# Kernel optimization log

Measured on AMD Instinct MI355X. Metric: run time of the kernel, lower is better.

## Reference

```python
import jax, jax.numpy as jnp
import numpy as np
from jax import lax

B, C, H, W = 2, 64, 192, 192
KS = 3
N = KS * KS
L = 3  # num_gdns (ResBlocks)


def conv2d(x, w, b=None, padding=0):
    out = lax.conv_general_dilated(x, w, (1, 1), [(padding, padding)] * 2,
                                   dimension_numbers=('NCHW', 'OIHW', 'NCHW'))
    if b is not None:
        out = out + b[None, :, None, None]
    return out


def gdn(x, beta, gamma):
    # y = x / sqrt(beta + sum_j gamma_ij x_j^2)  (inverse=False)
    norm = conv2d(x * x, gamma[:, :, None, None], beta)
    return x / jnp.sqrt(norm)


def resblock(x, w1, w2, beta, gamma):
    res = x
    h = jax.nn.celu(gdn(conv2d(x, w1, padding=0), beta, gamma))  # conv1: no pad (H-2)
    return conv2d(h, w2, padding=2) + res  # conv2: pad 2 restores H


def deform_conv(x, offset, w_dc):
    # DCNv1 (pure-pytorch impl): offset (b,2N,h,w), rows first then cols.
    b, c, Hh, Ww = x.shape
    h, w = offset.shape[2], offset.shape[3]
    pad = 1
    xp = jnp.pad(x, ((0, 0), (0, 0), (pad, pad), (pad, pad)))
    Hp, Wp = Hh + 2 * pad, Ww + 2 * pad
    r = (KS - 1) // 2
    knr, knc = jnp.meshgrid(jnp.arange(-r, r + 1), jnp.arange(-r, r + 1), indexing='ij')
    p_n = jnp.concatenate([knr.reshape(-1), knc.reshape(-1)]).astype(x.dtype)  # (2N,)
    gr, gc = jnp.meshgrid(jnp.arange(1, h + 1), jnp.arange(1, w + 1), indexing='ij')
    p0 = jnp.concatenate([jnp.broadcast_to(gr[None], (N, h, w)),
                          jnp.broadcast_to(gc[None], (N, h, w))], 0).astype(x.dtype)  # (2N,h,w)
    p = p0[None] + p_n[None, :, None, None] + offset  # (b,2N,h,w)
    p = jnp.transpose(p, (0, 2, 3, 1))  # (b,h,w,2N)
    pr = jnp.clip(p[..., :N], 0, Hp - 1)
    pc = jnp.clip(p[..., N:], 0, Wp - 1)
    q0 = lax.stop_gradient(jnp.floor(p))
    qr0 = jnp.clip(q0[..., :N], 0, Hp - 1).astype(jnp.int32)
    qc0 = jnp.clip(q0[..., N:], 0, Wp - 1).astype(jnp.int32)
    qr1 = jnp.clip(q0[..., :N] + 1, 0, Hp - 1).astype(jnp.int32)
    qc1 = jnp.clip(q0[..., N:] + 1, 0, Wp - 1).astype(jnp.int32)
    # bilinear weights (match torch impl exactly)
    g_lt = (1 + (qr0 - pr)) * (1 + (qc0 - pc))
    g_rb = (1 - (qr1 - pr)) * (1 - (qc1 - pc))
    g_lb = (1 + (qr0 - pr)) * (1 - (qc1 - pc))
    g_rt = (1 - (qr1 - pr)) * (1 + (qc0 - pc))
    xf = xp.reshape(b, c, Hp * Wp)

    def gather(qr, qc):
        idx = (qr * Wp + qc).reshape(b, -1)  # (b, h*w*N)
        g = jax.vmap(lambda xb, ib: xb[:, ib])(xf, idx)  # (b,c,h*w*N)
        return g.reshape(b, c, h, w, N)

    xo = (g_lt[:, None] * gather(qr0, qc0) + g_rb[:, None] * gather(qr1, qc1)
          + g_lb[:, None] * gather(qr0, qc1) + g_rt[:, None] * gather(qr1, qc0))
    # stride-ks conv over reshaped x_offset == contraction over (c, n)
    wf = w_dc.reshape(w_dc.shape[0], c, N)
    return jnp.einsum('bchwn,ocn->bohw', xo, wf)


def setup_inputs() -> dict:
    key = jax.random.key(0)
    ks = jax.random.split(key, 11)
    f_r = jax.random.normal(ks[0], (B, C, H, W), jnp.float32)
    m_t = jax.random.normal(ks[1], (B, C, H, W), jnp.float32)
    w_pconv = jax.random.normal(ks[2], (2 * N, C, KS, KS), jnp.float32) * 0.01
    b_pconv = jax.random.normal(ks[3], (2 * N,), jnp.float32) * 0.01
    w_dc = jax.random.normal(ks[4], (C, C, KS, KS), jnp.float32) * 0.05
    w_cat = jax.random.normal(ks[5], (C, 2 * C, KS, KS), jnp.float32) * 0.05
    b_cat = jax.random.normal(ks[6], (C,), jnp.float32) * 0.05
    rb_w1 = jax.random.normal(ks[7], (L, C, C, KS, KS), jnp.float32) * 0.01
    rb_w2 = jax.random.normal(ks[8], (L, C, C, KS, KS), jnp.float32) * 0.01
    rb_beta = jax.random.uniform(ks[9], (L, C), jnp.float32) * 0.5 + 0.5
    rb_gamma = jnp.broadcast_to(0.1 * jnp.eye(C, dtype=jnp.float32), (L, C, C)) \
        + jax.random.uniform(ks[10], (L, C, C), jnp.float32) * 0.01
    return {"f_r": f_r, "m_t": m_t, "w_pconv": w_pconv, "b_pconv": b_pconv,
            "w_dc": w_dc, "w_cat": w_cat, "b_cat": b_cat,
            "rb_w1": rb_w1, "rb_w2": rb_w2, "rb_beta": rb_beta, "rb_gamma": rb_gamma}


def reference(f_r, m_t, w_pconv, b_pconv, w_dc, w_cat, b_cat, rb_w1, rb_w2, rb_beta, rb_gamma):
    offset = conv2d(m_t, w_pconv, b_pconv, padding=1)  # (B, 2N, H, W)
    x = deform_conv(f_r, offset, w_dc)                  # (B, C, H, W)
    y = conv2d(jnp.concatenate([x, f_r], axis=1), w_cat, b_cat, padding=1)
    for i in range(L):
        y = resblock(y, rb_w1[i], rb_w2[i], rb_beta[i], rb_gamma[i])
    return y + x
```

## Files before the change

kernel.cpp:

```cpp
#include <hip/hip_runtime.h>

typedef __attribute__((ext_vector_type(8))) __bf16 bf16x8;
typedef __attribute__((ext_vector_type(4))) __bf16 bf16x4;
typedef __attribute__((ext_vector_type(16))) float f32x16;
typedef __attribute__((ext_vector_type(4))) float f32x4;
typedef __attribute__((ext_vector_type(4))) int i32x4;

#define HH 192
#define WW 192
#define HW 36864
#define HW1 36100

#define TCS 144
#define RP66 (66 * TCS)
#define RPA (34 * TCS)
#define RPB (36 * TCS)
#define LDSA (4 * RPA)
#define LDSB (6 * RPB)
#define GDNPITCH 144
#define TREG 8704

__device__ inline f32x16 mfma32(bf16x8 a, bf16x8 b, f32x16 c) {
  return __builtin_amdgcn_mfma_f32_32x32x16_bf16(a, b, c, 0, 0, 0);
}

__device__ inline f32x16 zero16() {
  f32x16 z;
#pragma unroll
  for (int e = 0; e < 16; ++e) z[e] = 0.f;
  return z;
}

__global__ __launch_bounds__(256) void prep_weights(
    const float* __restrict__ wp, const float* __restrict__ bp,
    const float* __restrict__ wdc, const float* __restrict__ wcat,
    const float* __restrict__ w1, const float* __restrict__ w2,
    const float* __restrict__ gamma,
    __bf16* __restrict__ wpA, __bf16* __restrict__ wdcA,
    __bf16* __restrict__ wcatA, __bf16* __restrict__ w1A,
    __bf16* __restrict__ w2A, __bf16* __restrict__ gA,
    float* __restrict__ bpad) {
  int i = blockIdx.x * 256 + threadIdx.x;
  if (i < 18432) {
    int j = i & 7, lane = (i >> 3) & 63, kc = (i >> 9) & 3, n = i >> 11;
    int o = lane & 31, c = kc * 16 + ((lane >> 5) << 3) + j;
    wpA[i] = (o < 18) ? (__bf16)wp[(o * 64 + c) * 9 + n] : (__bf16)0.f;
    return;
  }
  i -= 18432;
  if (i < 36864) {
    int j = i & 7, lane = (i >> 3) & 63, ot = (i >> 9) & 1, kc = (i >> 10) & 3, n = i >> 12;
    int o = ot * 32 + (lane & 31), c = kc * 16 + ((lane >> 5) << 3) + j;
    wdcA[i] = (__bf16)wdc[(o * 64 + c) * 9 + n];
    return;
  }
  i -= 36864;
  if (i < 73728) {
    int d = i, j = d & 7; d >>= 3; int lane = d & 63; d >>= 6; int ot = d & 1; d >>= 1;
    int kc = d & 7; int n = d >> 3;
    int o = ot * 32 + (lane & 31), c = kc * 16 + ((lane >> 5) << 3) + j;
    wcatA[i] = (__bf16)wcat[(o * 128 + c) * 9 + n];
    return;
  }
  i -= 73728;
  if (i < 110592) {
    int l = i / 36864, di = i % 36864, d = di;
    int j = d & 7; d >>= 3; int lane = d & 63; d >>= 6; int ot = d & 1; d >>= 1;
    int kc = d & 3; int n = d >> 2;
    int o = ot * 32 + (lane & 31), c = kc * 16 + ((lane >> 5) << 3) + j;
    w1A[l * 36864 + di] = (__bf16)w1[l * 36864 + (o * 64 + c) * 9 + n];
    return;
  }
  i -= 110592;
  if (i < 110592) {
    int l = i / 36864, di = i % 36864, d = di;
    int j = d & 7; d >>= 3; int lane = d & 63; d >>= 6; int ot = d & 1; d >>= 1;
    int kc = d & 3; int n = d >> 2;
    int o = ot * 32 + (lane & 31), c = kc * 16 + ((lane >> 5) << 3) + j;
    w2A[l * 36864 + di] = (__bf16)w2[l * 36864 + (o * 64 + c) * 9 + n];
    return;
  }
  i -= 110592;
  if (i < 12288) {
    int l = i / 4096, di = i % 4096, d = di;
    int j = d & 7; d >>= 3; int lane = d & 63; d >>= 6; int ot = d & 1; d >>= 1;
    int kc = d & 3;
    int o = ot * 32 + (lane & 31), c = kc * 16 + ((lane >> 5) << 3) + j;
    gA[l * 4096 + di] = (__bf16)gamma[l * 4096 + o * 64 + c];
    return;
  }
  i -= 12288;
  if (i < 20) bpad[i] = (i < 18) ? bp[i] : 0.f;
}

__global__ __launch_bounds__(256) void to_nhwc_bf16(
    const float* __restrict__ fr, const float* __restrict__ mt,
    __bf16* __restrict__ frn, __bf16* __restrict__ mtn) {
  __shared__ __align__(16) __bf16 tile[64 * 72];
  int tensor = blockIdx.x / 1152, rem = blockIdx.x % 1152;
  int b = rem / 576, p0 = (rem % 576) * 64;
  const float* src = (tensor ? mt : fr) + (size_t)b * 64 * HW;
  __bf16* dst = (tensor ? mtn : frn) + (size_t)b * HW * 64;
  int tid = threadIdx.x, c = tid >> 2, q0 = (tid & 3) * 16;
  const float* sp = src + (size_t)c * HW + p0 + q0;
#pragma unroll
  for (int qq = 0; qq < 4; ++qq) {
    f32x4 v = *(const f32x4*)(sp + qq * 4);
#pragma unroll
    for (int e = 0; e < 4; ++e) tile[(q0 + qq * 4 + e) * 72 + c] = (__bf16)v[e];
  }
  __syncthreads();
  int px = tid >> 2, c0 = (tid & 3) * 16;
  bf16x8 a = *(const bf16x8*)(&tile[px * 72 + c0]);
  bf16x8 b8 = *(const bf16x8*)(&tile[px * 72 + c0 + 8]);
  __bf16* dp = dst + (size_t)(p0 + px) * 64 + c0;
  *(bf16x8*)dp = a;
  *(bf16x8*)(dp + 8) = b8;
}

template <int ROWS, int COLS, int TPB>
__device__ inline void stage_f32T(const float* __restrict__ src,
                                  int srcH, int srcW, int row0, int col0,
                                  unsigned char* lds) {
  for (int i = threadIdx.x; i < ROWS * COLS * 16; i += TPB) {
    int r = i / (COLS * 16), rem = i - r * (COLS * 16), j = rem >> 4, q = rem & 15;
    int gr = row0 + r, gc = col0 + j;
    f32x4 v = {0.f, 0.f, 0.f, 0.f};
    if (gr >= 0 && gr < srcH && gc >= 0 && gc < srcW)
      v = *(const f32x4*)(src + ((size_t)gr * srcW + gc) * 64 + q * 4);
    bf16x4 o;
#pragma unroll
    for (int e = 0; e < 4; ++e) o[e] = (__bf16)v[e];
    *(bf16x4*)(lds + r * (COLS * TCS) + j * TCS + q * 8) = o;
  }
}

template <int ROWS, int COLS, int TPB>
__device__ inline void stage_bf16T(const __bf16* __restrict__ src,
                                   int srcH, int srcW, int row0, int col0,
                                   unsigned char* lds) {
  for (int i = threadIdx.x; i < ROWS * COLS * 8; i += TPB) {
    int r = i / (COLS * 8), rem = i - r * (COLS * 8), j = rem >> 3, u = rem & 7;
    int gr = row0 + r, gc = col0 + j;
    bf16x8 v;
#pragma unroll
    for (int e = 0; e < 8; ++e) v[e] = (__bf16)0.f;
    if (gr >= 0 && gr < srcH && gc >= 0 && gc < srcW)
      v = *(const bf16x8*)(src + ((size_t)gr * srcW + gc) * 64 + u * 8);
    *(bf16x8*)(lds + r * (COLS * TCS) + j * TCS + u * 16) = v;
  }
}

template <int KC, int KOFFA, int RP>
__device__ inline void kloopW(const __bf16* __restrict__ wA,
                              const unsigned char* __restrict__ bB,
                              int ot, f32x16 acc2[2]) {
  const int lane = threadIdx.x & 63;
  const __bf16* aB = wA + lane * 8;
#pragma unroll
  for (int n = 0; n < 9; ++n) {
    const int kh = n / 3, kw = n % 3;
#pragma unroll
    for (int kc = 0; kc < 4; ++kc) {
      bf16x8 a = *(const bf16x8*)(aB + ((n * KC + KOFFA + kc) * 2 + ot) * 512);
      bf16x8 b0 = *(const bf16x8*)(bB + kh * RP + kw * TCS + kc * 32);
      acc2[kc & 1] = mfma32(a, b0, acc2[kc & 1]);
    }
  }
}

__device__ inline void acc32_to_lds(const f32x16 acc[2], unsigned char* reg) {
  int lane = threadIdx.x & 63;
  int colb = lane & 31, half = lane >> 5;
#pragma unroll
  for (int ot = 0; ot < 2; ++ot)
#pragma unroll
    for (int g = 0; g < 4; ++g) {
      int o = ot * 32 + half * 4 + g * 8;
      f32x4 v;
      v[0] = acc[ot][g * 4 + 0]; v[1] = acc[ot][g * 4 + 1];
      v[2] = acc[ot][g * 4 + 2]; v[3] = acc[ot][g * 4 + 3];
      *(f32x4*)(reg + (colb * 68 + o) * 4) = v;
    }
}

__global__ __launch_bounds__(256, 1) void pconv_mfma(
    const __bf16* __restrict__ mtn, const __bf16* __restrict__ wpA,
    const float* __restrict__ bpad, float* __restrict__ off20) {
  __shared__ __align__(16) unsigned char smem[6 * RP66];
  int b = blockIdx.x / 144, r = blockIdx.x % 144, rt = r / 3, ct = r % 3;
  int h0 = rt * 4, w0 = ct * 64;
  int wid = threadIdx.x >> 6, lane = threadIdx.x & 63;
  int colb = lane & 31, half = lane >> 5, kh8 = half << 3;
  stage_bf16T<6, 66, 256>(mtn + (size_t)b * HW * 64, 192, 192, h0 - 1, w0 - 1, smem);
  const __bf16* aB = wpA + lane * 8;
  bf16x8 pcur[4], pnxt[4];
#pragma unroll
  for (int kc = 0; kc < 4; ++kc) pcur[kc] = *(const bf16x8*)(aB + kc * 512);
  __syncthreads();
  f32x16 acc[2];
  acc[0] = zero16(); acc[1] = zero16();
  {
    const unsigned char* bB = smem + wid * RP66 + colb * TCS + kh8 * 2;
#pragma unroll
    for (int n = 0; n < 9; ++n) {
      if (n < 8) {
#pragma unroll
        for (int kc = 0; kc < 4; ++kc)
          pnxt[kc] = *(const bf16x8*)(aB + ((n + 1) * 4 + kc) * 512);
      }
      const int kh = n / 3, kw = n % 3;
#pragma unroll
      for (int kc = 0; kc < 4; ++kc) {
        const unsigned char* bp = bB + kh * RP66 + kw * TCS + kc * 32;
        bf16x8 b0 = *(const bf16x8*)(bp);
        bf16x8 b1 = *(const bf16x8*)(bp + 32 * TCS);
        acc[0] = mfma32(pcur[kc], b0, acc[0]);
        acc[1] = mfma32(pcur[kc], b1, acc[1]);
      }
#pragma unroll
      for (int kc = 0; kc < 4; ++kc) pcur[kc] = pnxt[kc];
    }
  }
  __syncthreads();
  unsigned char* reg = smem + wid * 9216;
#pragma unroll
  for (int pt = 0; pt < 2; ++pt)
#pragma unroll
    for (int g = 0; g < 4; ++g) {
      int o = half * 4 + g * 8;
      f32x4 v;
      v[0] = acc[pt][g * 4 + 0]; v[1] = acc[pt][g * 4 + 1];
      v[2] = acc[pt][g * 4 + 2]; v[3] = acc[pt][g * 4 + 3];
      *(f32x4*)(reg + ((pt * 32 + colb) * 36 + o) * 4) = v;
    }
  __builtin_amdgcn_s_waitcnt(0);
  size_t pix = (size_t)b * HW + (size_t)(h0 + wid) * 192 + w0 + lane;
#pragma unroll
  for (int q = 0; q < 5; ++q) {
    f32x4 v = *(const f32x4*)(reg + (lane * 36 + q * 4) * 4);
    v += *(const f32x4*)(bpad + q * 4);
    *(f32x4*)(off20 + pix * 20 + q * 4) = v;
  }
}

#define GOPITCH 32
#define DTBL (9 * 32 * GOPITCH)
#define DBUF 4608
#define DLDS (DTBL + 2 * DBUF)
__global__ __launch_bounds__(128, 2) void deform_mfma(
    const __bf16* __restrict__ frn, const float* __restrict__ off20,
    const __bf16* __restrict__ wdcA, float* __restrict__ xlow) {
  __shared__ __align__(16) unsigned char smem[DLDS];
  int bid = (blockIdx.x & 7) * 288 + (blockIdx.x >> 3);
  int b = bid / 1152, r = bid % 1152;
  int h = r / 6, s = r % 6;
  int w0 = s * 32;
  int tid = threadIdx.x;
  int wid = tid >> 6, lane = tid & 63;
  int m = lane & 31, half = lane >> 5;
  int pxg = lane >> 3, slot = lane & 7;
  const __bf16* xb = frn + (size_t)b * HW * 64;
  {
    int px = tid & 31, g = tid >> 5;
    int w = w0 + px;
    size_t pixl = (size_t)b * HW + (size_t)h * 192 + w;
    const float* ofp = off20 + pixl * 20;
    for (int n = g; n < 9; n += 4) {
      float offr = ofp[n], offc = ofp[9 + n];
      float pr = (float)(h + 1 + n / 3 - 1) + offr;
      float pc = (float)(w + 1 + n % 3 - 1) + offc;
      float prc = fminf(fmaxf(pr, 0.f), 193.f);
      float pcc = fminf(fmaxf(pc, 0.f), 193.f);
      float f0r = floorf(pr), f0c = floorf(pc);
      int qr0 = (int)fminf(fmaxf(f0r, 0.f), 193.f);
      int qc0 = (int)fminf(fmaxf(f0c, 0.f), 193.f);
      int qr1 = (int)fminf(fmaxf(f0r + 1.f, 0.f), 193.f);
      int qc1 = (int)fminf(fmaxf(f0c + 1.f, 0.f), 193.f);
      float dr0 = 1.f + ((float)qr0 - prc);
      float dr1 = 1.f - ((float)qr1 - prc);
      float dc0 = 1.f + ((float)qc0 - pcc);
      float dc1 = 1.f - ((float)qc1 - pcc);
      int o0, o1, o2, o3; float g0, g1, g2, g3;
      { bool v = (qr0 >= 1 && qr0 <= 192 && qc0 >= 1 && qc0 <= 192);
        o0 = min(max(qr0-1,0),191)*WW + min(max(qc0-1,0),191); g0 = v ? dr0*dc0 : 0.f; }
      { bool v = (qr1 >= 1 && qr1 <= 192 && qc1 >= 1 && qc1 <= 192);
        o1 = min(max(qr1-1,0),191)*WW + min(max(qc1-1,0),191); g1 = v ? dr1*dc1 : 0.f; }
      { bool v = (qr0 >= 1 && qr0 <= 192 && qc1 >= 1 && qc1 <= 192);
        o2 = min(max(qr0-1,0),191)*WW + min(max(qc1-1,0),191); g2 = v ? dr0*dc1 : 0.f; }
      { bool v = (qr1 >= 1 && qr1 <= 192 && qc0 >= 1 && qc0 <= 192);
        o3 = min(max(qr1-1,0),191)*WW + min(max(qc0-1,0),191); g3 = v ? dr1*dc0 : 0.f; }
      unsigned char* dst = smem + (n * 32 + px) * GOPITCH;
      f32x4 gv; gv[0] = g0; gv[1] = g1; gv[2] = g2; gv[3] = g3;
      i32x4 ov; ov[0] = o0; ov[1] = o1; ov[2] = o2; ov[3] = o3;
      *(f32x4*)dst = gv;
      *(i32x4*)(dst + 16) = ov;
    }
  }
  __syncthreads();
  f32x16 acc[2];
  acc[0] = zero16(); acc[1] = zero16();
  const __bf16* aB = wdcA + lane * 8;
  unsigned char* buf = smem + DTBL + wid * DBUF;
  const unsigned char* bB = buf + m * TCS + (half << 3) * 2;
  int n0 = wid ? 0 : 5, nn = wid ? 5 : 4;

  bf16x8 C[4][4];
  f32x4 G[4];
  bf16x8 a[8];

  auto load_tap = [&](int n) {
#pragma unroll
    for (int i = 0; i < 4; ++i) {
      const unsigned char* gp = smem + (size_t)(n * 32 + i * 8 + pxg) * GOPITCH;
      i32x4 oi = *(const i32x4*)(gp + 16);
      G[i] = *(const f32x4*)gp;
#pragma unroll
      for (int j = 0; j < 4; ++j)
        C[i][j] = *(const bf16x8*)(xb + (size_t)oi[j] * 64 + slot * 8);
    }
  };
  auto load_a = [&](int n) {
#pragma unroll
    for (int kc = 0; kc < 4; ++kc) {
      a[kc * 2 + 0] = *(const bf16x8*)(aB + ((n * 4 + kc) * 2 + 0) * 512);
      a[kc * 2 + 1] = *(const bf16x8*)(aB + ((n * 4 + kc) * 2 + 1) * 512);
    }
  };
  auto blend_write = [&]() {
#pragma unroll
    for (int i = 0; i < 4; ++i) {
      bf16x8 ov;
#pragma unroll
      for (int e = 0; e < 8; ++e) {
        float f = G[i][0] * (float)C[i][0][e] + G[i][1] * (float)C[i][1][e] +
                  G[i][2] * (float)C[i][2][e] + G[i][3] * (float)C[i][3][e];
        ov[e] = (__bf16)f;
      }
      *(bf16x8*)(buf + (i * 8 + pxg) * TCS + slot * 16) = ov;
    }
  };
  auto consume = [&]() {
#pragma unroll
    for (int kc = 0; kc < 4; ++kc) {
      bf16x8 b0 = *(const bf16x8*)(bB + kc * 32);
      acc[0] = mfma32(a[kc * 2 + 0], b0, acc[0]);
      acc[1] = mfma32(a[kc * 2 + 1], b0, acc[1]);
    }
  };

  load_tap(n0);
  blend_write();
  for (int t = 1; t < nn; ++t) {
    load_a(n0 + t - 1);
    load_tap(n0 + t);
    consume();
    asm volatile("s_waitcnt lgkmcnt(0)" ::: "memory");
    blend_write();
  }
  load_a(n0 + nn - 1);
  consume();
  __syncthreads();
  unsigned char* reg = smem;
  if (wid == 1) acc32_to_lds(acc, reg);
  __syncthreads();
  if (wid == 0) {
    int colb = m;
#pragma unroll
    for (int ot = 0; ot < 2; ++ot)
#pragma unroll
      for (int g = 0; g < 4; ++g) {
        int o = ot * 32 + half * 4 + g * 8;
        f32x4 v = *(const f32x4*)(reg + (colb * 68 + o) * 4);
        v[0] += acc[ot][g * 4 + 0]; v[1] += acc[ot][g * 4 + 1];
        v[2] += acc[ot][g * 4 + 2]; v[3] += acc[ot][g * 4 + 3];
        *(f32x4*)(reg + (colb * 68 + o) * 4) = v;
      }
    __builtin_amdgcn_s_waitcnt(0);
    int ch = half * 32;
    float* dp = xlow + ((size_t)b * HW + (size_t)h * 192 + w0 + colb) * 64 + ch;
#pragma unroll
    for (int q = 0; q < 8; ++q)
      *(f32x4*)(dp + q * 4) = *(const f32x4*)(reg + (colb * 68 + ch + q * 4) * 4);
  }
}

__global__ __launch_bounds__(256, 1) void convcat_mfma(
    const float* __restrict__ xlow, const __bf16* __restrict__ frn,
    const __bf16* __restrict__ wA, const float* __restrict__ bias,
    __bf16* __restrict__ y) {
  __shared__ __align__(16) unsigned char smem[LDSA];
  int b = blockIdx.x / 576, r = blockIdx.x % 576, rt = r / 6, ct = r % 6;
  int h0 = rt * 2, w0 = ct * 32;
  int tid = threadIdx.x;
  int wid = tid >> 6, lane = tid & 63;
  int pt = wid & 1, ot = wid >> 1;
  int m = lane & 31, half = lane >> 5, kh8 = half << 3;
  const unsigned char* bB = smem + pt * RPA + m * TCS + kh8 * 2;
  f32x16 acc2[2];
  acc2[0] = zero16(); acc2[1] = zero16();
  stage_f32T<4, 34, 256>(xlow + (size_t)b * HW * 64, 192, 192, h0 - 1, w0 - 1, smem);
  __syncthreads();
  kloopW<8, 0, RPA>(wA, bB, ot, acc2);
  __syncthreads();
  stage_bf16T<4, 34, 256>(frn + (size_t)b * HW * 64, 192, 192, h0 - 1, w0 - 1, smem);
  __syncthreads();
  kloopW<8, 4, RPA>(wA, bB, ot, acc2);
  __syncthreads();
  f32x16 acc = acc2[0] + acc2[1];
  unsigned char* reg = smem + pt * TREG;
#pragma unroll
  for (int g = 0; g < 4; ++g) {
    int o = ot * 32 + half * 4 + g * 8;
    f32x4 v;
    v[0] = acc[g * 4 + 0]; v[1] = acc[g * 4 + 1];
    v[2] = acc[g * 4 + 2]; v[3] = acc[g * 4 + 3];
    *(f32x4*)(reg + (m * 68 + o) * 4) = v;
  }
  __syncthreads();
  int ch = ot * 32 + half * 16;
  int row = h0 + pt;
  __bf16* dp = y + ((size_t)b * HW + (size_t)row * 192 + w0 + m) * 64 + ch;
#pragma unroll
  for (int q = 0; q < 4; ++q) {
    f32x4 v = *(const f32x4*)(reg + (m * 68 + ch + q * 4) * 4);
    v += *(const f32x4*)(bias + ch + q * 4);
    bf16x4 o8;
#pragma unroll
    for (int e = 0; e < 4; ++e) o8[e] = (__bf16)v[e];
    *(bf16x4*)(dp + q * 4) = o8;
  }
}

__global__ __launch_bounds__(256, 1) void conv1gdn_mfma(
    const __bf16* __restrict__ y, const __bf16* __restrict__ w1A,
    const __bf16* __restrict__ gA, const float* __restrict__ beta,
    __bf16* __restrict__ hbuf) {
  __shared__ __align__(16) unsigned char smem[LDSA];
  int b = blockIdx.x / 576, r = blockIdx.x % 576, rt = r / 6, ct = r % 6;
  int h0 = rt * 2, w0 = ct * 32;
  int tid = threadIdx.x;
  int wid = tid >> 6, lane = tid & 63;
  int pt = wid & 1, ot = wid >> 1;
  int m = lane & 31, half = lane >> 5, kh8 = half << 3;
  const unsigned char* bB = smem + pt * RPA + m * TCS + kh8 * 2;
  f32x16 acc2[2];
  acc2[0] = zero16(); acc2[1] = zero16();
  stage_bf16T<4, 34, 256>(y + (size_t)b * HW * 64, 192, 192, h0, w0, smem);
  __syncthreads();
  kloopW<4, 0, RPA>(w1A, bB, ot, acc2);
  __syncthreads();
  f32x16 acc = acc2[0] + acc2[1];
  unsigned char* gdnreg = smem;
  {
    int p = pt * 32 + m;
#pragma unroll
    for (int g = 0; g < 4; ++g) {
      int o = ot * 32 + half * 4 + g * 8;
      bf16x4 s;
#pragma unroll
      for (int e = 0; e < 4; ++e) {
        float x = acc[g * 4 + e];
        s[e] = (__bf16)(x * x);
      }
      *(bf16x4*)(gdnreg + p * GDNPITCH + o * 2) = s;
    }
  }
  __syncthreads();
  f32x16 nacc = zero16();
  {
    const __bf16* gaB = gA + lane * 8;
    const unsigned char* gb = gdnreg + (pt * 32 + m) * GDNPITCH + kh8 * 2;
#pragma unroll
    for (int kc = 0; kc < 4; ++kc) {
      bf16x8 ga = *(const bf16x8*)(gaB + (kc * 2 + ot) * 512);
      bf16x8 b0 = *(const bf16x8*)(gb + kc * 32);
      nacc = mfma32(ga, b0, nacc);
    }
  }
#pragma unroll
  for (int g = 0; g < 4; ++g) {
    f32x4 bet = *(const f32x4*)(beta + ot * 32 + half * 4 + g * 8);
#pragma unroll
    for (int e = 0; e < 4; ++e) {
      float nv = bet[e] + nacc[g * 4 + e];
      float hv = acc[g * 4 + e] * rsqrtf(nv);
      hv = hv > 0.f ? hv : expf(hv) - 1.f;
      acc[g * 4 + e] = hv;
    }
  }
  __syncthreads();
  unsigned char* reg = smem + pt * TREG;
#pragma unroll
  for (int g = 0; g < 4; ++g) {
    int o = ot * 32 + half * 4 + g * 8;
    f32x4 v;
    v[0] = acc[g * 4 + 0]; v[1] = acc[g * 4 + 1];
    v[2] = acc[g * 4 + 2]; v[3] = acc[g * 4 + 3];
    *(f32x4*)(reg + (m * 68 + o) * 4) = v;
  }
  __syncthreads();
  int ch = ot * 32 + half * 16;
  int hr = h0 + pt, wcol = w0 + m;
  if (hr < 190 && wcol < 190) {
    __bf16* dp = hbuf + ((size_t)b * HW1 + (size_t)hr * 190 + wcol) * 64 + ch;
#pragma unroll
    for (int q = 0; q < 4; ++q) {
      f32x4 v = *(const f32x4*)(reg + (m * 68 + ch + q * 4) * 4);
      bf16x4 o8;
#pragma unroll
      for (int e = 0; e < 4; ++e) o8[e] = (__bf16)v[e];
      *(bf16x4*)(dp + q * 4) = o8;
    }
  }
}

template <bool LAST>
__global__ __launch_bounds__(256, 1) void conv2_mfma(
    const __bf16* __restrict__ hbuf, const __bf16* __restrict__ w2A,
    const float* __restrict__ xlow, __bf16* __restrict__ y,
    float* __restrict__ out) {
  __shared__ __align__(16) unsigned char smem[LDSB];
  int b = blockIdx.x / 576, r = blockIdx.x % 576, rt = r / 6, ct = r % 6;
  int h0 = rt * 2, w0 = ct * 32;
  int tid = threadIdx.x;
  int wid = tid >> 6, lane = tid & 63;
  int pt = wid & 1, ot = wid >> 1;
  int m = lane & 31, half = lane >> 5, kh8 = half << 3;
  const unsigned char* bB = smem + pt * RPB + m * TCS + kh8 * 2;
  f32x16 acc2[2];
  acc2[0] = zero16(); acc2[1] = zero16();
  stage_bf16T<6, 36, 256>(hbuf + (size_t)b * HW1 * 64, 190, 190, h0 - 2, w0 - 2, smem);
  __syncthreads();
  kloopW<4, 0, RPB>(w2A, bB, ot, acc2);
  __syncthreads();
  f32x16 acc = acc2[0] + acc2[1];
  unsigned char* reg = smem + pt * TREG;
#pragma unroll
  for (int g = 0; g < 4; ++g) {
    int o = ot * 32 + half * 4 + g * 8;
    f32x4 v;
    v[0] = acc[g * 4 + 0]; v[1] = acc[g * 4 + 1];
    v[2] = acc[g * 4 + 2]; v[3] = acc[g * 4 + 3];
    *(f32x4*)(reg + (m * 68 + o) * 4) = v;
  }
  __syncthreads();
  int ch = ot * 32 + half * 16;
  int row = h0 + pt;
  size_t pix = (size_t)b * HW + (size_t)row * 192 + w0 + m;
  __bf16* yp = y + pix * 64 + ch;
  f32x4 v[4];
#pragma unroll
  for (int q = 0; q < 4; ++q) {
    v[q] = *(const f32x4*)(reg + (m * 68 + ch + q * 4) * 4);
    bf16x4 yv = *(const bf16x4*)(yp + q * 4);
#pragma unroll
    for (int e = 0; e < 4; ++e) v[q][e] += (float)yv[e];
  }
  if (!LAST) {
#pragma unroll
    for (int q = 0; q < 4; ++q) {
      bf16x4 o8;
#pragma unroll
      for (int e = 0; e < 4; ++e) o8[e] = (__bf16)v[q][e];
      *(bf16x4*)(yp + q * 4) = o8;
    }
  } else {
    const float* xp = xlow + pix * 64 + ch;
#pragma unroll
    for (int q = 0; q < 4; ++q) v[q] += *(const f32x4*)(xp + q * 4);
#pragma unroll
    for (int q = 0; q < 4; ++q)
      *(f32x4*)(reg + (m * 68 + ch + q * 4) * 4) = v[q];
    __syncthreads();
    int o = lane;
    float* op = out + ((size_t)b * 64 + o) * HW + (size_t)row * 192 + w0;
#pragma unroll
    for (int qq = 0; qq < 4; ++qq) {
      int q = ot * 4 + qq;
      f32x4 s;
#pragma unroll
      for (int e = 0; e < 4; ++e)
        s[e] = *(const float*)(reg + ((q * 4 + e) * 68 + o) * 4);
      *(f32x4*)(op + q * 4) = s;
    }
  }
}

extern "C" void kernel_launch(void* const* d_in, const int* in_sizes, int n_in,
                              void* d_out, int out_size, void* d_ws, size_t ws_size,
                              hipStream_t stream) {
  const float* f_r      = (const float*)d_in[0];
  const float* m_t      = (const float*)d_in[1];
  const float* w_pconv  = (const float*)d_in[2];
  const float* b_pconv  = (const float*)d_in[3];
  const float* w_dc     = (const float*)d_in[4];
  const float* w_cat    = (const float*)d_in[5];
  const float* b_cat    = (const float*)d_in[6];
  const float* rb_w1    = (const float*)d_in[7];
  const float* rb_w2    = (const float*)d_in[8];
  const float* rb_beta  = (const float*)d_in[9];
  const float* rb_gamma = (const float*)d_in[10];
  float* out = (float*)d_out;

  float* ws = (float*)d_ws;
  float*  xlow  = ws;
  __bf16* ybuf  = (__bf16*)(xlow + 4718592);
  float*  off20 = xlow + 4718592 + 4718592;
  __bf16* frn   = (__bf16*)(off20 + 1474560);
  __bf16* mtn   = (__bf16*)(off20 + 1474560 + 2359296);
  __bf16* hbuf  = mtn;
  float*  wbase = off20 + 1474560 + 2359296 + 2359296;
  __bf16* wpA   = (__bf16*)wbase;
  __bf16* wdcA  = (__bf16*)(wbase + 9216);
  __bf16* wcatA = (__bf16*)(wbase + 27648);
  __bf16* w1A   = (__bf16*)(wbase + 64512);
  __bf16* w2A   = (__bf16*)(wbase + 119808);
  __bf16* gA    = (__bf16*)(wbase + 175104);
  float*  bpad  = wbase + 181248;

  prep_weights<<<1417, 256, 0, stream>>>(w_pconv, b_pconv, w_dc, w_cat, rb_w1, rb_w2,
                                         rb_gamma, wpA, wdcA, wcatA, w1A, w2A, gA, bpad);
  to_nhwc_bf16<<<2304, 256, 0, stream>>>(f_r, m_t, frn, mtn);
  pconv_mfma<<<288, 256, 0, stream>>>(mtn, wpA, bpad, off20);
  deform_mfma<<<2304, 128, 0, stream>>>(frn, off20, wdcA, xlow);
  convcat_mfma<<<1152, 256, 0, stream>>>(xlow, frn, wcatA, b_cat, ybuf);
  for (int l = 0; l < 3; ++l) {
    conv1gdn_mfma<<<1152, 256, 0, stream>>>(ybuf, w1A + l * 36864, gA + l * 4096,
                                            rb_beta + l * 64, hbuf);
    if (l < 2)
      conv2_mfma<false><<<1152, 256, 0, stream>>>(hbuf, w2A + l * 36864, xlow, ybuf, out);
    else
      conv2_mfma<true><<<1152, 256, 0, stream>>>(hbuf, w2A + l * 36864, xlow, ybuf, out);
  }
}
```

Baseline: 292.8 us.

## Stage conv tiles via global_load_lds with XOR swizzle and split-K wave groups

The conv kernels (convcat, conv1gdn, conv2) now stage input rows straight into LDS with global_load_lds, using an XOR-swizzled layout and a zero-pad buffer for out-of-bounds pixels. The work split changes so each wave computes two output rows and one output-channel half. The two wave groups split the taps or input-channel halves and their partial sums are merged through LDS. Deform also writes a bf16 copy of its output, so convcat no longer stages and converts fp32, and occupancy hints rise to two blocks per CU. The intent is to cut staging latency and conversion cost and to reuse weight fragments, at the cost of an extra merge pass, extra bf16 writes and idle waves during the epilogue.

Result: faster. 274.4 us (-6.3%).

```diff
diff --git a/kernel.cpp b/kernel.cpp
--- a/kernel.cpp
+++ b/kernel.cpp
@@ -13,12 +13,9 @@
 
 #define TCS 144
 #define RP66 (66 * TCS)
-#define RPA (34 * TCS)
-#define RPB (36 * TCS)
-#define LDSA (4 * RPA)
-#define LDSB (6 * RPB)
 #define GDNPITCH 144
 #define TREG 8704
+#define TROW 5120
 
 __device__ inline f32x16 mfma32(bf16x8 a, bf16x8 b, f32x16 c) {
   return __builtin_amdgcn_mfma_f32_32x32x16_bf16(a, b, c, 0, 0, 0);
@@ -90,7 +87,7 @@
     return;
   }
   i -= 12288;
-  if (i < 20) bpad[i] = (i < 18) ? bp[i] : 0.f;
+  if (i < 96) bpad[i] = (i < 18) ? bp[i] : 0.f;
 }
 
 __global__ __launch_bounds__(256) void to_nhwc_bf16(
@@ -119,23 +116,6 @@
 }
 
 template <int ROWS, int COLS, int TPB>
-__device__ inline void stage_f32T(const float* __restrict__ src,
-                                  int srcH, int srcW, int row0, int col0,
-                                  unsigned char* lds) {
-  for (int i = threadIdx.x; i < ROWS * COLS * 16; i += TPB) {
-    int r = i / (COLS * 16), rem = i - r * (COLS * 16), j = rem >> 4, q = rem & 15;
-    int gr = row0 + r, gc = col0 + j;
-    f32x4 v = {0.f, 0.f, 0.f, 0.f};
-    if (gr >= 0 && gr < srcH && gc >= 0 && gc < srcW)
-      v = *(const f32x4*)(src + ((size_t)gr * srcW + gc) * 64 + q * 4);
-    bf16x4 o;
-#pragma unroll
-    for (int e = 0; e < 4; ++e) o[e] = (__bf16)v[e];
-    *(bf16x4*)(lds + r * (COLS * TCS) + j * TCS + q * 8) = o;
-  }
-}
-
-template <int ROWS, int COLS, int TPB>
 __device__ inline void stage_bf16T(const __bf16* __restrict__ src,
                                    int srcH, int srcW, int row0, int col0,
                                    unsigned char* lds) {
@@ -151,21 +131,81 @@
   }
 }
 
-template <int KC, int KOFFA, int RP>
-__device__ inline void kloopW(const __bf16* __restrict__ wA,
-                              const unsigned char* __restrict__ bB,
-                              int ot, f32x16 acc2[2]) {
-  const int lane = threadIdx.x & 63;
-  const __bf16* aB = wA + lane * 8;
-#pragma unroll
-  for (int n = 0; n < 9; ++n) {
-    const int kh = n / 3, kw = n % 3;
-#pragma unroll
-    for (int kc = 0; kc < 4; ++kc) {
-      bf16x8 a = *(const bf16x8*)(aB + ((n * KC + KOFFA + kc) * 2 + ot) * 512);
-      bf16x8 b0 = *(const bf16x8*)(bB + kh * RP + kw * TCS + kc * 32);
-      acc2[kc & 1] = mfma32(a, b0, acc2[kc & 1]);
-    }
+__device__ inline void stage_glds(const __bf16* __restrict__ src, int H, int W,
+                                  int gr, int gc0, const __bf16* __restrict__ zpad,
+                                  unsigned char* ldsrow, int chunk) {
+  int l = threadIdx.x & 63;
+  int colg = l >> 3, gsrc = (l & 7) ^ colg;
+  int gc = gc0 + chunk * 8 + colg;
+  const __bf16* gp = zpad;
+  if (gr >= 0 && gr < H && gc >= 0 && gc < W)
+    gp = src + ((size_t)gr * W + gc) * 64 + gsrc * 8;
+  __builtin_amdgcn_global_load_lds(
+      (const __attribute__((address_space(1))) void*)gp,
+      (__attribute__((address_space(3))) void*)(ldsrow + chunk * 1024), 16, 0, 0);
+}
+
+template <int KCW>
+__device__ inline void tapG(const __bf16* __restrict__ aB, int ot,
+                            const unsigned char* __restrict__ tile,
+                            int n, int koff, f32x16 acc[2]) {
+  int lane = threadIdx.x & 63;
+  int m = lane & 31, half = lane >> 5;
+  int kh = n / 3, kw = n % 3;
+  int p = kw + m, p7 = p & 7;
+  bf16x8 A[4], B0[4], B1[4];
+#pragma unroll
+  for (int kc = 0; kc < 4; ++kc)
+    A[kc] = *(const bf16x8*)(aB + (size_t)((n * KCW + koff + kc) * 2 + ot) * 512);
+#pragma unroll
+  for (int kc = 0; kc < 4; ++kc) {
+    int gsl = ((kc * 2 + half) ^ p7) << 4;
+    B0[kc] = *(const bf16x8*)(tile + (kh + 0) * TROW + p * 128 + gsl);
+    B1[kc] = *(const bf16x8*)(tile + (kh + 1) * TROW + p * 128 + gsl);
+  }
+#pragma unroll
+  for (int kc = 0; kc < 4; ++kc) {
+    acc[0] = mfma32(A[kc], B0[kc], acc[0]);
+    acc[1] = mfma32(A[kc], B1[kc], acc[1]);
+  }
+}
+
+__device__ inline void merge_write(const f32x16 acc[2], unsigned char* mb) {
+  int l = threadIdx.x & 63;
+  unsigned char* p = mb + l * 128;
+#pragma unroll
+  for (int pt = 0; pt < 2; ++pt)
+#pragma unroll
+    for (int i = 0; i < 4; ++i) {
+      f32x4 v;
+      v[0] = acc[pt][i * 4 + 0]; v[1] = acc[pt][i * 4 + 1];
+      v[2] = acc[pt][i * 4 + 2]; v[3] = acc[pt][i * 4 + 3];
+      *(f32x4*)(p + (((pt * 4 + i) ^ (l & 7)) * 16)) = v;
+    }
+}
+__device__ inline void merge_add(f32x16 acc[2], const unsigned char* mb) {
+  int l = threadIdx.x & 63;
+  const unsigned char* p = mb + l * 128;
+#pragma unroll
+  for (int pt = 0; pt < 2; ++pt)
+#pragma unroll
+    for (int i = 0; i < 4; ++i) {
+      f32x4 v = *(const f32x4*)(p + (((pt * 4 + i) ^ (l & 7)) * 16));
+      acc[pt][i * 4 + 0] += v[0]; acc[pt][i * 4 + 1] += v[1];
+      acc[pt][i * 4 + 2] += v[2]; acc[pt][i * 4 + 3] += v[3];
+    }
+}
+
+__device__ inline void treg_write(const f32x16& a, int ot, unsigned char* reg) {
+  int lane = threadIdx.x & 63;
+  int m = lane & 31, half = lane >> 5;
+#pragma unroll
+  for (int g = 0; g < 4; ++g) {
+    int o = ot * 32 + half * 4 + g * 8;
+    f32x4 v;
+    v[0] = a[g * 4 + 0]; v[1] = a[g * 4 + 1];
+    v[2] = a[g * 4 + 2]; v[3] = a[g * 4 + 3];
+    *(f32x4*)(reg + (m * 68 + o) * 4) = v;
   }
 }
 
@@ -250,7 +290,8 @@
 #define DLDS (DTBL + 2 * DBUF)
 __global__ __launch_bounds__(128, 2) void deform_mfma(
     const __bf16* __restrict__ frn, const float* __restrict__ off20,
-    const __bf16* __restrict__ wdcA, float* __restrict__ xlow) {
+    const __bf16* __restrict__ wdcA, float* __restrict__ xlow,
+    __bf16* __restrict__ xlowb) {
   __shared__ __align__(16) unsigned char smem[DLDS];
   int bid = (blockIdx.x & 7) * 288 + (blockIdx.x >> 3);
   int b = bid / 1152, r = bid % 1152;
@@ -378,211 +419,243 @@
       }
     __builtin_amdgcn_s_waitcnt(0);
     int ch = half * 32;
-    float* dp = xlow + ((size_t)b * HW + (size_t)h * 192 + w0 + colb) * 64 + ch;
-#pragma unroll
-    for (int q = 0; q < 8; ++q)
-      *(f32x4*)(dp + q * 4) = *(const f32x4*)(reg + (colb * 68 + ch + q * 4) * 4);
-  }
-}
-
-__global__ __launch_bounds__(256, 1) void convcat_mfma(
-    const float* __restrict__ xlow, const __bf16* __restrict__ frn,
+    size_t pix = (size_t)b * HW + (size_t)h * 192 + w0 + colb;
+    float* dp = xlow + pix * 64 + ch;
+    __bf16* dpb = xlowb + pix * 64 + ch;
+#pragma unroll
+    for (int q = 0; q < 8; ++q) {
+      f32x4 v = *(const f32x4*)(reg + (colb * 68 + ch + q * 4) * 4);
+      *(f32x4*)(dp + q * 4) = v;
+      bf16x4 o8;
+#pragma unroll
+      for (int e = 0; e < 4; ++e) o8[e] = (__bf16)v[e];
+      *(bf16x4*)(dpb + q * 4) = o8;
+    }
+  }
+}
+
+__global__ __launch_bounds__(256, 2) void convcat_mfma(
+    const __bf16* __restrict__ xlowb, const __bf16* __restrict__ frn,
     const __bf16* __restrict__ wA, const float* __restrict__ bias,
-    __bf16* __restrict__ y) {
-  __shared__ __align__(16) unsigned char smem[LDSA];
-  int b = blockIdx.x / 576, r = blockIdx.x % 576, rt = r / 6, ct = r % 6;
+    const __bf16* __restrict__ zpad, __bf16* __restrict__ y) {
+  __shared__ __align__(16) unsigned char smem[2 * 4 * TROW];
+  int bid = (blockIdx.x & 7) * 144 + (blockIdx.x >> 3);
+  int b = bid / 576, r = bid % 576, rt = r / 6, ct = r % 6;
   int h0 = rt * 2, w0 = ct * 32;
-  int tid = threadIdx.x;
-  int wid = tid >> 6, lane = tid & 63;
-  int pt = wid & 1, ot = wid >> 1;
-  int m = lane & 31, half = lane >> 5, kh8 = half << 3;
-  const unsigned char* bB = smem + pt * RPA + m * TCS + kh8 * 2;
-  f32x16 acc2[2];
-  acc2[0] = zero16(); acc2[1] = zero16();
-  stage_f32T<4, 34, 256>(xlow + (size_t)b * HW * 64, 192, 192, h0 - 1, w0 - 1, smem);
-  __syncthreads();
-  kloopW<8, 0, RPA>(wA, bB, ot, acc2);
-  __syncthreads();
-  stage_bf16T<4, 34, 256>(frn + (size_t)b * HW * 64, 192, 192, h0 - 1, w0 - 1, smem);
-  __syncthreads();
-  kloopW<8, 4, RPA>(wA, bB, ot, acc2);
-  __syncthreads();
-  f32x16 acc = acc2[0] + acc2[1];
-  unsigned char* reg = smem + pt * TREG;
-#pragma unroll
-  for (int g = 0; g < 4; ++g) {
-    int o = ot * 32 + half * 4 + g * 8;
-    f32x4 v;
-    v[0] = acc[g * 4 + 0]; v[1] = acc[g * 4 + 1];
-    v[2] = acc[g * 4 + 2]; v[3] = acc[g * 4 + 3];
-    *(f32x4*)(reg + (m * 68 + o) * 4) = v;
-  }
-  __syncthreads();
-  int ch = ot * 32 + half * 16;
-  int row = h0 + pt;
-  __bf16* dp = y + ((size_t)b * HW + (size_t)row * 192 + w0 + m) * 64 + ch;
-#pragma unroll
-  for (int q = 0; q < 4; ++q) {
-    f32x4 v = *(const f32x4*)(reg + (m * 68 + ch + q * 4) * 4);
-    v += *(const f32x4*)(bias + ch + q * 4);
-    bf16x4 o8;
-#pragma unroll
-    for (int e = 0; e < 4; ++e) o8[e] = (__bf16)v[e];
-    *(bf16x4*)(dp + q * 4) = o8;
-  }
-}
-
-__global__ __launch_bounds__(256, 1) void conv1gdn_mfma(
+  int tid = threadIdx.x, wid = tid >> 6, lane = tid & 63;
+  int ot = wid & 1, g = wid >> 1;
+  int m = lane & 31, half = lane >> 5;
+  const __bf16* src0 = xlowb + (size_t)b * HW * 64;
+  const __bf16* src1 = frn + (size_t)b * HW * 64;
+  for (int o = wid; o < 40; o += 4) {
+    int t = o / 20, rr = (o % 20) / 5, ck = o % 5;
+    stage_glds(t ? src1 : src0, 192, 192, h0 - 1 + rr, w0 - 1, zpad,
+               smem + t * (4 * TROW) + rr * TROW, ck);
+  }
+  __syncthreads();
+  const __bf16* aB = wA + lane * 8;
+  const unsigned char* tile = smem + g * (4 * TROW);
+  int koff = g ? 4 : 0;
+  f32x16 acc[2];
+  acc[0] = zero16(); acc[1] = zero16();
+#pragma unroll
+  for (int n = 0; n < 9; ++n) tapG<8>(aB, ot, tile, n, koff, acc);
+  __syncthreads();
+  if (g == 1) merge_write(acc, smem + ot * 8192);
+  __syncthreads();
+  if (g == 0) merge_add(acc, smem + ot * 8192);
+  __syncthreads();
+  if (g == 0) {
+    treg_write(acc[0], ot, smem);
+    treg_write(acc[1], ot, smem + TREG);
+  }
+  __syncthreads();
+  if (g == 0) {
+    const unsigned char* reg = smem + ot * TREG;
+    int ch = half * 32;
+    int row = h0 + ot;
+    __bf16* dp = y + ((size_t)b * HW + (size_t)row * 192 + w0 + m) * 64 + ch;
+#pragma unroll
+    for (int q = 0; q < 8; ++q) {
+      f32x4 v = *(const f32x4*)(reg + (m * 68 + ch + q * 4) * 4);
+      v += *(const f32x4*)(bias + ch + q * 4);
+      bf16x4 o8;
+#pragma unroll
+      for (int e = 0; e < 4; ++e) o8[e] = (__bf16)v[e];
+      *(bf16x4*)(dp + q * 4) = o8;
+    }
+  }
+}
+
+__global__ __launch_bounds__(256, 2) void conv1gdn_mfma(
     const __bf16* __restrict__ y, const __bf16* __restrict__ w1A,
     const __bf16* __restrict__ gA, const float* __restrict__ beta,
-    __bf16* __restrict__ hbuf) {
-  __shared__ __align__(16) unsigned char smem[LDSA];
-  int b = blockIdx.x / 576, r = blockIdx.x % 576, rt = r / 6, ct = r % 6;
+    const __bf16* __restrict__ zpad, __bf16* __restrict__ hbuf) {
+  __shared__ __align__(16) unsigned char smem[9216 + 2 * TREG];
+  int bid = (blockIdx.x & 7) * 144 + (blockIdx.x >> 3);
+  int b = bid / 576, r = bid % 576, rt = r / 6, ct = r % 6;
   int h0 = rt * 2, w0 = ct * 32;
-  int tid = threadIdx.x;
-  int wid = tid >> 6, lane = tid & 63;
-  int pt = wid & 1, ot = wid >> 1;
+  int tid = threadIdx.x, wid = tid >> 6, lane = tid & 63;
+  int ot = wid & 1, g = wid >> 1;
   int m = lane & 31, half = lane >> 5, kh8 = half << 3;
-  const unsigned char* bB = smem + pt * RPA + m * TCS + kh8 * 2;
-  f32x16 acc2[2];
-  acc2[0] = zero16(); acc2[1] = zero16();
-  stage_bf16T<4, 34, 256>(y + (size_t)b * HW * 64, 192, 192, h0, w0, smem);
-  __syncthreads();
-  kloopW<4, 0, RPA>(w1A, bB, ot, acc2);
-  __syncthreads();
-  f32x16 acc = acc2[0] + acc2[1];
+  const __bf16* src = y + (size_t)b * HW * 64;
+  for (int o = wid; o < 20; o += 4) {
+    int rr = o / 5, ck = o % 5;
+    stage_glds(src, 192, 192, h0 + rr, w0, zpad, smem + rr * TROW, ck);
+  }
+  __syncthreads();
+  const __bf16* aB = w1A + lane * 8;
+  f32x16 acc[2];
+  acc[0] = zero16(); acc[1] = zero16();
+  int n0 = g ? 5 : 0, nn = g ? 4 : 5;
+  for (int t = 0; t < nn; ++t) tapG<4>(aB, ot, smem, n0 + t, 0, acc);
+  __syncthreads();
+  if (g == 1) merge_write(acc, smem + ot * 8192);
+  __syncthreads();
+  if (g == 0) merge_add(acc, smem + ot * 8192);
+  __syncthreads();
   unsigned char* gdnreg = smem;
-  {
-    int p = pt * 32 + m;
-#pragma unroll
-    for (int g = 0; g < 4; ++g) {
-      int o = ot * 32 + half * 4 + g * 8;
-      bf16x4 s;
-#pragma unroll
-      for (int e = 0; e < 4; ++e) {
-        float x = acc[g * 4 + e];
-        s[e] = (__bf16)(x * x);
+  if (g == 0) {
+#pragma unroll
+    for (int pt = 0; pt < 2; ++pt)
+#pragma unroll
+      for (int gg = 0; gg < 4; ++gg) {
+        int o = ot * 32 + half * 4 + gg * 8;
+        int p = pt * 32 + m;
+        bf16x4 s;
+#pragma unroll
+        for (int e = 0; e < 4; ++e) {
+          float x = acc[pt][gg * 4 + e];
+          s[e] = (__bf16)(x * x);
+        }
+        *(bf16x4*)(gdnreg + p * GDNPITCH + o * 2) = s;
       }
-      *(bf16x4*)(gdnreg + p * GDNPITCH + o * 2) = s;
-    }
-  }
-  __syncthreads();
-  f32x16 nacc = zero16();
-  {
+  }
+  __syncthreads();
+  if (g == 0) {
+    f32x16 nacc[2];
+    nacc[0] = zero16(); nacc[1] = zero16();
     const __bf16* gaB = gA + lane * 8;
-    const unsigned char* gb = gdnreg + (pt * 32 + m) * GDNPITCH + kh8 * 2;
+    const unsigned char* gb = gdnreg + m * GDNPITCH + kh8 * 2;
 #pragma unroll
     for (int kc = 0; kc < 4; ++kc) {
       bf16x8 ga = *(const bf16x8*)(gaB + (kc * 2 + ot) * 512);
       bf16x8 b0 = *(const bf16x8*)(gb + kc * 32);
-      nacc = mfma32(ga, b0, nacc);
-    }
-  }
-#pragma unroll
-  for (int g = 0; g < 4; ++g) {
-    f32x4 bet = *(const f32x4*)(beta + ot * 32 + half * 4 + g * 8);
-#pragma unroll
-    for (int e = 0; e < 4; ++e) {
-      float nv = bet[e] + nacc[g * 4 + e];
-      float hv = acc[g * 4 + e] * rsqrtf(nv);
-      hv = hv > 0.f ? hv : expf(hv) - 1.f;
-      acc[g * 4 + e] = hv;
-    }
-  }
-  __syncthreads();
-  unsigned char* reg = smem + pt * TREG;
-#pragma unroll
-  for (int g = 0; g < 4; ++g) {
-    int o = ot * 32 + half * 4 + g * 8;
-    f32x4 v;
-    v[0] = acc[g * 4 + 0]; v[1] = acc[g * 4 + 1];
-    v[2] = acc[g * 4 + 2]; v[3] = acc[g * 4 + 3];
-    *(f32x4*)(reg + (m * 68 + o) * 4) = v;
-  }
-  __syncthreads();
-  int ch = ot * 32 + half * 16;
-  int hr = h0 + pt, wcol = w0 + m;
-  if (hr < 190 && wcol < 190) {
-    __bf16* dp = hbuf + ((size_t)b * HW1 + (size_t)hr * 190 + wcol) * 64 + ch;
-#pragma unroll
-    for (int q = 0; q < 4; ++q) {
-      f32x4 v = *(const f32x4*)(reg + (m * 68 + ch + q * 4) * 4);
-      bf16x4 o8;
-#pragma unroll
-      for (int e = 0; e < 4; ++e) o8[e] = (__bf16)v[e];
-      *(bf16x4*)(dp + q * 4) = o8;
+      bf16x8 b1 = *(const bf16x8*)(gb + 32 * GDNPITCH + kc * 32);
+      nacc[0] = mfma32(ga, b0, nacc[0]);
+      nacc[1] = mfma32(ga, b1, nacc[1]);
+    }
+#pragma unroll
+    for (int gg = 0; gg < 4; ++gg) {
+      f32x4 bet = *(const f32x4*)(beta + ot * 32 + half * 4 + gg * 8);
+#pragma unroll
+      for (int pt = 0; pt < 2; ++pt)
+#pragma unroll
+        for (int e = 0; e < 4; ++e) {
+          float nv = bet[e] + nacc[pt][gg * 4 + e];
+          float hv = acc[pt][gg * 4 + e] * rsqrtf(nv);
+          hv = hv > 0.f ? hv : expf(hv) - 1.f;
+          acc[pt][gg * 4 + e] = hv;
+        }
+    }
+  }
+  __syncthreads();
+  if (g == 0) {
+    treg_write(acc[0], ot, smem);
+    treg_write(acc[1], ot, smem + TREG);
+  }
+  __syncthreads();
+  if (g == 0) {
+    const unsigned char* reg = smem + ot * TREG;
+    int ch = half * 32;
+    int hr = h0 + ot, wcol = w0 + m;
+    if (hr < 190 && wcol < 190) {
+      __bf16* dp = hbuf + ((size_t)b * HW1 + (size_t)hr * 190 + wcol) * 64 + ch;
+#pragma unroll
+      for (int q = 0; q < 8; ++q) {
+        f32x4 v = *(const f32x4*)(reg + (m * 68 + ch + q * 4) * 4);
+        bf16x4 o8;
+#pragma unroll
+        for (int e = 0; e < 4; ++e) o8[e] = (__bf16)v[e];
+        *(bf16x4*)(dp + q * 4) = o8;
+      }
     }
   }
 }
 
 template <bool LAST>
-__global__ __launch_bounds__(256, 1) void conv2_mfma(
+__global__ __launch_bounds__(256, 2) void conv2_mfma(
     const __bf16* __restrict__ hbuf, const __bf16* __restrict__ w2A,
-    const float* __restrict__ xlow, __bf16* __restrict__ y,
-    float* __restrict__ out) {
-  __shared__ __align__(16) unsigned char smem[LDSB];
-  int b = blockIdx.x / 576, r = blockIdx.x % 576, rt = r / 6, ct = r % 6;
+    const float* __restrict__ xlow, const __bf16* __restrict__ zpad,
+    __bf16* __restrict__ y, float* __restrict__ out) {
+  __shared__ __align__(16) unsigned char smem[4 * TROW];
+  int bid = (blockIdx.x & 7) * 144 + (blockIdx.x >> 3);
+  int b = bid / 576, r = bid % 576, rt = r / 6, ct = r % 6;
   int h0 = rt * 2, w0 = ct * 32;
-  int tid = threadIdx.x;
-  int wid = tid >> 6, lane = tid & 63;
-  int pt = wid & 1, ot = wid >> 1;
-  int m = lane & 31, half = lane >> 5, kh8 = half << 3;
-  const unsigned char* bB = smem + pt * RPB + m * TCS + kh8 * 2;
-  f32x16 acc2[2];
-  acc2[0] = zero16(); acc2[1] = zero16();
-  stage_bf16T<6, 36, 256>(hbuf + (size_t)b * HW1 * 64, 190, 190, h0 - 2, w0 - 2, smem);
-  __syncthreads();
-  kloopW<4, 0, RPB>(w2A, bB, ot, acc2);
-  __syncthreads();
-  f32x16 acc = acc2[0] + acc2[1];
-  unsigned char* reg = smem + pt * TREG;
-#pragma unroll
-  for (int g = 0; g < 4; ++g) {
-    int o = ot * 32 + half * 4 + g * 8;
-    f32x4 v;
-    v[0] = acc[g * 4 + 0]; v[1] = acc[g * 4 + 1];
-    v[2] = acc[g * 4 + 2]; v[3] = acc[g * 4 + 3];
-    *(f32x4*)(reg + (m * 68 + o) * 4) = v;
-  }
-  __syncthreads();
-  int ch = ot * 32 + half * 16;
-  int row = h0 + pt;
-  size_t pix = (size_t)b * HW + (size_t)row * 192 + w0 + m;
-  __bf16* yp = y + pix * 64 + ch;
-  f32x4 v[4];
-#pragma unroll
-  for (int q = 0; q < 4; ++q) {
-    v[q] = *(const f32x4*)(reg + (m * 68 + ch + q * 4) * 4);
-    bf16x4 yv = *(const bf16x4*)(yp + q * 4);
-#pragma unroll
-    for (int e = 0; e < 4; ++e) v[q][e] += (float)yv[e];
-  }
-  if (!LAST) {
-#pragma unroll
-    for (int q = 0; q < 4; ++q) {
-      bf16x4 o8;
-#pragma unroll
-      for (int e = 0; e < 4; ++e) o8[e] = (__bf16)v[q][e];
-      *(bf16x4*)(yp + q * 4) = o8;
-    }
-  } else {
-    const float* xp = xlow + pix * 64 + ch;
-#pragma unroll
-    for (int q = 0; q < 4; ++q) v[q] += *(const f32x4*)(xp + q * 4);
-#pragma unroll
-    for (int q = 0; q < 4; ++q)
-      *(f32x4*)(reg + (m * 68 + ch + q * 4) * 4) = v[q];
-    __syncthreads();
-    int o = lane;
-    float* op = out + ((size_t)b * 64 + o) * HW + (size_t)row * 192 + w0;
-#pragma unroll
-    for (int qq = 0; qq < 4; ++qq) {
-      int q = ot * 4 + qq;
-      f32x4 s;
-#pragma unroll
-      for (int e = 0; e < 4; ++e)
-        s[e] = *(const float*)(reg + ((q * 4 + e) * 68 + o) * 4);
-      *(f32x4*)(op + q * 4) = s;
+  int tid = threadIdx.x, wid = tid >> 6, lane = tid & 63;
+  int ot = wid & 1, g = wid >> 1;
+  int m = lane & 31, half = lane >> 5;
+  const __bf16* src = hbuf + (size_t)b * HW1 * 64;
+  for (int o = wid; o < 20; o += 4) {
+    int rr = o / 5, ck = o % 5;
+    stage_glds(src, 190, 190, h0 - 2 + rr, w0 - 2, zpad, smem + rr * TROW, ck);
+  }
+  __syncthreads();
+  const __bf16* aB = w2A + lane * 8;
+  f32x16 acc[2];
+  acc[0] = zero16(); acc[1] = zero16();
+  int n0 = g ? 5 : 0, nn = g ? 4 : 5;
+  for (int t = 0; t < nn; ++t) tapG<4>(aB, ot, smem, n0 + t, 0, acc);
+  __syncthreads();
+  if (g == 1) merge_write(acc, smem + ot * 8192);
+  __syncthreads();
+  if (g == 0) merge_add(acc, smem + ot * 8192);
+  __syncthreads();
+  if (g == 0) {
+    treg_write(acc[0], ot, smem);
+    treg_write(acc[1], ot, smem + TREG);
+  }
+  __syncthreads();
+  if (g == 0) {
+    unsigned char* reg = smem + ot * TREG;
+    int ch = half * 32;
+    int row = h0 + ot;
+    size_t pix = (size_t)b * HW + (size_t)row * 192 + w0 + m;
+    __bf16* yp = y + pix * 64 + ch;
+    f32x4 v[8];
+#pragma unroll
+    for (int q = 0; q < 8; ++q) {
+      v[q] = *(const f32x4*)(reg + (m * 68 + ch + q * 4) * 4);
+      bf16x4 yv = *(const bf16x4*)(yp + q * 4);
+#pragma unroll
+      for (int e = 0; e < 4; ++e) v[q][e] += (float)yv[e];
+    }
+    if (!LAST) {
+#pragma unroll
+      for (int q = 0; q < 8; ++q) {
+        bf16x4 o8;
+#pragma unroll
+        for (int e = 0; e < 4; ++e) o8[e] = (__bf16)v[q][e];
+        *(bf16x4*)(yp + q * 4) = o8;
+      }
+    } else {
+      const float* xp = xlow + pix * 64 + ch;
+#pragma unroll
+      for (int q = 0; q < 8; ++q) v[q] += *(const f32x4*)(xp + q * 4);
+#pragma unroll
+      for (int q = 0; q < 8; ++q)
+        *(f32x4*)(reg + (m * 68 + ch + q * 4) * 4) = v[q];
+      __builtin_amdgcn_s_waitcnt(0);
+      int o = lane;
+      float* op = out + ((size_t)b * 64 + o) * HW + (size_t)row * 192 + w0;
+#pragma unroll
+      for (int q = 0; q < 8; ++q) {
+        f32x4 s;
+#pragma unroll
+        for (int e = 0; e < 4; ++e)
+          s[e] = *(const float*)(reg + ((q * 4 + e) * 68 + o) * 4);
+        *(f32x4*)(op + q * 4) = s;
+      }
     }
   }
 }
@@ -606,6 +679,7 @@
   float* ws = (float*)d_ws;
   float*  xlow  = ws;
   __bf16* ybuf  = (__bf16*)(xlow + 4718592);
+  __bf16* xlowb = (__bf16*)(xlow + 4718592 + 2359296);
   float*  off20 = xlow + 4718592 + 4718592;
   __bf16* frn   = (__bf16*)(off20 + 1474560);
   __bf16* mtn   = (__bf16*)(off20 + 1474560 + 2359296);
@@ -618,19 +692,20 @@
   __bf16* w2A   = (__bf16*)(wbase + 119808);
   __bf16* gA    = (__bf16*)(wbase + 175104);
   float*  bpad  = wbase + 181248;
+  const __bf16* zpad = (const __bf16*)(bpad + 32);
 
   prep_weights<<<1417, 256, 0, stream>>>(w_pconv, b_pconv, w_dc, w_cat, rb_w1, rb_w2,
                                          rb_gamma, wpA, wdcA, wcatA, w1A, w2A, gA, bpad);
   to_nhwc_bf16<<<2304, 256, 0, stream>>>(f_r, m_t, frn, mtn);
   pconv_mfma<<<288, 256, 0, stream>>>(mtn, wpA, bpad, off20);
-  deform_mfma<<<2304, 128, 0, stream>>>(frn, off20, wdcA, xlow);
-  convcat_mfma<<<1152, 256, 0, stream>>>(xlow, frn, wcatA, b_cat, ybuf);
+  deform_mfma<<<2304, 128, 0, stream>>>(frn, off20, wdcA, xlow, xlowb);
+  convcat_mfma<<<1152, 256, 0, stream>>>(xlowb, frn, wcatA, b_cat, zpad, ybuf);
   for (int l = 0; l < 3; ++l) {
     conv1gdn_mfma<<<1152, 256, 0, stream>>>(ybuf, w1A + l * 36864, gA + l * 4096,
-                                            rb_beta + l * 64, hbuf);
+                                            rb_beta + l * 64, zpad, hbuf);
     if (l < 2)
-      conv2_mfma<false><<<1152, 256, 0, stream>>>(hbuf, w2A + l * 36864, xlow, ybuf, out);
+      conv2_mfma<false><<<1152, 256, 0, stream>>>(hbuf, w2A + l * 36864, xlow, zpad, ybuf, out);
     else
-      conv2_mfma<true><<<1152, 256, 0, stream>>>(hbuf, w2A + l * 36864, xlow, ybuf, out);
-  }
-}
+      conv2_mfma<true><<<1152, 256, 0, stream>>>(hbuf, w2A + l * 36864, xlow, zpad, ybuf, out);
+  }
+}
```
